# Kernel optimization log

Measured on AMD Instinct MI355X. Metric: run time of the kernel, lower is better.

The kernel has to match this reference:

```python
import jax, jax.numpy as jnp
import numpy as np

IN_FEATURES = 2048
OUT_FEATURES = 8192


def setup_inputs() -> dict:
    key = jax.random.key(0)
    k_x, k_w, k_s, k_b = jax.random.split(key, 4)
    x = jax.random.normal(k_x, (4, 2048, IN_FEATURES), dtype=jnp.float32)
    # int8 weights as produced by quantize(): values in [-128, 127]
    weight_int8 = jax.random.randint(k_w, (OUT_FEATURES, IN_FEATURES), -128, 128, dtype=jnp.int8)
    # per-output-row scale, shape [out_features, 1]
    scale = jax.random.uniform(k_s, (OUT_FEATURES, 1), dtype=jnp.float32, minval=1e-4, maxval=0.02)
    bias = jax.random.normal(k_b, (OUT_FEATURES,), dtype=jnp.float32) * 0.01
    return {"x": x, "weight_int8": weight_int8, "scale": scale, "bias": bias}


def reference(x, weight_int8, scale, bias):
    # dequantize: [out, in] int8 -> x.dtype, scaled per output row
    weight = weight_int8.astype(x.dtype) * scale.astype(x.dtype)
    # F.linear: x @ weight.T + bias
    return jnp.einsum('bsi,oi->bso', x, weight) + bias.astype(x.dtype)
```

## Files before the change

kernel.cpp:

```cpp
#include <hip/hip_runtime.h>
#include <hip/hip_bf16.h>

#define M_DIM 8192
#define N_DIM 8192
#define K_DIM 2048

#define BK 64
#define NT (K_DIM / BK)
#define SLOT_BYTES 32768

typedef float f32x4 __attribute__((ext_vector_type(4)));
typedef int   i32x4 __attribute__((ext_vector_type(4)));
typedef unsigned int u32;
typedef u32 u32x2 __attribute__((ext_vector_type(2)));
typedef u32 u32x4 __attribute__((ext_vector_type(4)));


__device__ __forceinline__ void gload16(const unsigned char* g, char* l) {
    __builtin_amdgcn_global_load_lds(
        (const __attribute__((address_space(1))) u32*)g,
        (__attribute__((address_space(3))) u32*)l, 16, 0, 0);
}

__device__ __forceinline__ u32 pack4(int a, int b, int c, int d) {
    return (u32)(a & 255) | ((u32)(b & 255) << 8) |
           ((u32)(c & 255) << 16) | ((u32)(d & 255) << 24);
}


__global__ void __launch_bounds__(256) quant_x_k(const float* __restrict__ x,
                                                 unsigned char* __restrict__ xq,
                                                 float* __restrict__ sx) {
    const int row = blockIdx.x;
    const int t = threadIdx.x;
    const float* xr = x + (size_t)row * K_DIM;
    f32x4 v0 = *((const f32x4*)xr + t * 2);
    f32x4 v1 = *((const f32x4*)xr + t * 2 + 1);
    float m = fabsf(v0[0]);
    m = fmaxf(m, fabsf(v0[1])); m = fmaxf(m, fabsf(v0[2])); m = fmaxf(m, fabsf(v0[3]));
    m = fmaxf(m, fabsf(v1[0])); m = fmaxf(m, fabsf(v1[1]));
    m = fmaxf(m, fabsf(v1[2])); m = fmaxf(m, fabsf(v1[3]));
#pragma unroll
    for (int off = 32; off >= 1; off >>= 1)
        m = fmaxf(m, __shfl_xor(m, off, 64));
    __shared__ float wmax[4];
    if ((t & 63) == 0) wmax[t >> 6] = m;
    __syncthreads();
    m = fmaxf(fmaxf(wmax[0], wmax[1]), fmaxf(wmax[2], wmax[3]));
    m = fmaxf(m, 1e-20f);
    const float rs = 127.0f / m;
    const int q0 = (int)rintf(v0[0] * rs), q1 = (int)rintf(v0[1] * rs);
    const int q2 = (int)rintf(v0[2] * rs), q3 = (int)rintf(v0[3] * rs);
    const int q4 = (int)rintf(v1[0] * rs), q5 = (int)rintf(v1[1] * rs);
    const int q6 = (int)rintf(v1[2] * rs), q7 = (int)rintf(v1[3] * rs);
    u32x2 o;
    o[0] = pack4(q0, q1, q2, q3);
    o[1] = pack4(q4, q5, q6, q7);
    *((u32x2*)(xq + (size_t)row * K_DIM) + t) = o;
    if (t == 0) sx[row] = m / 127.0f;
}


__global__ void __launch_bounds__(256) cvt_w_k(const int* __restrict__ w,
                                               unsigned char* __restrict__ wq, int n16) {
    const int stride = gridDim.x * blockDim.x;
    for (int i = blockIdx.x * blockDim.x + threadIdx.x; i < n16; i += stride) {
        const i32x4* p = (const i32x4*)w + (size_t)i * 4;
        i32x4 a = p[0], b = p[1], c = p[2], d = p[3];
        u32x4 o;
        o[0] = pack4(a[0], a[1], a[2], a[3]);
        o[1] = pack4(b[0], b[1], b[2], b[3]);
        o[2] = pack4(c[0], c[1], c[2], c[3]);
        o[3] = pack4(d[0], d[1], d[2], d[3]);
        *((u32x4*)wq + i) = o;
    }
}


__global__ void __launch_bounds__(512, 2)
gemm_i8(const unsigned char* __restrict__ Aq, const unsigned char* __restrict__ Bq,
        const float* __restrict__ sx, const float* __restrict__ sw,
        const float* __restrict__ bias, float* __restrict__ C) {
    extern __shared__ __align__(16) char ldsb[];

    const int bid = blockIdx.x;
    const int swz = (bid & 7) * 128 + (bid >> 3);
    const int rowBase = (swz >> 5) * 256;
    const int colBase = (swz & 31) * 256;

    const int t = threadIdx.x;
    const int l = t & 63;
    const int w = t >> 6;
    const int wm = w >> 2;
    const int wn = w & 3;
    const int fr = l & 15;
    const int s4 = l >> 4;

    const int sr = t >> 2;
    const int sk = (((t & 3) ^ ((sr >> 1) & 3)) * 16);
    const unsigned char* gA0 = Aq + (size_t)(rowBase + sr) * K_DIM + sk;
    const unsigned char* gA1 = Aq + (size_t)(rowBase + 128 + sr) * K_DIM + sk;
    const unsigned char* gB0 = Bq + (size_t)(colBase + sr) * K_DIM + sk;
    const unsigned char* gB1 = Bq + (size_t)(colBase + 128 + sr) * K_DIM + sk;

#define STAGE(tk) do { \
        char* _b = ldsb + ((tk) & 3) * SLOT_BYTES; \
        const int _k = (tk) * BK; \
        gload16(gA0 + _k, _b + t * 16); \
        gload16(gA1 + _k, _b + 8192 + t * 16); \
        gload16(gB0 + _k, _b + 16384 + t * 16); \
        gload16(gB1 + _k, _b + 24576 + t * 16); \
    } while (0)

    const int pc = ((s4 ^ ((fr >> 1) & 3)) * 16);
    int aoff[8], boff[4];
#pragma unroll
    for (int mi = 0; mi < 8; ++mi)
        aoff[mi] = (wm * 128 + mi * 16 + fr) * 64 + pc;
#pragma unroll
    for (int ni = 0; ni < 4; ++ni)
        boff[ni] = 16384 + (wn * 64 + ni * 16 + fr) * 64 + pc;

    i32x4 acc[8][4] = {};
    i32x4 af0[8], bf0[4], af1[8], bf1[4];

#define SB    __builtin_amdgcn_sched_barrier(0)
#define BAR   __builtin_amdgcn_s_barrier()
#define P1    __builtin_amdgcn_s_setprio(1)
#define P0    __builtin_amdgcn_s_setprio(0)
#define LGKM0 asm volatile("s_waitcnt lgkmcnt(0)" ::: "memory")
#define VM4   asm volatile("s_waitcnt vmcnt(4)" ::: "memory")
#define VM0   asm volatile("s_waitcnt vmcnt(0)" ::: "memory")

#define READS(T, AF, BF) do { \
        const char* _s = ldsb + ((T) & 3) * SLOT_BYTES; \
        _Pragma("unroll") \
        for (int mi = 0; mi < 8; ++mi) AF[mi] = *(const i32x4*)(_s + aoff[mi]); \
        _Pragma("unroll") \
        for (int ni = 0; ni < 4; ++ni) BF[ni] = *(const i32x4*)(_s + boff[ni]); \
    } while (0)

#define MFMA32(AF, BF) do { P1; \
        _Pragma("unroll") \
        for (int mi = 0; mi < 8; ++mi) \
            _Pragma("unroll") \
            for (int ni = 0; ni < 4; ++ni) \
                acc[mi][ni] = __builtin_amdgcn_mfma_i32_16x16x64_i8( \
                    AF[mi], BF[ni], acc[mi][ni], 0, 0, 0); \
        P0; } while (0)

#define BODY(T, AC, BC, AN, BN, DOSTAGE, VMW) do { \
        READS(T, AN, BN); \
        if (DOSTAGE) STAGE((T) + 2); \
        SB; \
        MFMA32(AC, BC); \
        VMW; LGKM0; SB; BAR; SB; \
    } while (0)

    STAGE(0); STAGE(1); STAGE(2);
    VM4; SB; BAR; SB;
    READS(0, af0, bf0);
    LGKM0; SB;

#pragma unroll
    for (int tt = 1; tt <= 27; tt += 2) {
        BODY(tt,     af0, bf0, af1, bf1, true, VM4);
        BODY(tt + 1, af1, bf1, af0, bf0, true, VM4);
    }
    BODY(29, af0, bf0, af1, bf1, true,  VM4);
    BODY(30, af1, bf1, af0, bf0, false, VM0);
    READS(31, af1, bf1);
    SB;
    MFMA32(af0, bf0);
    LGKM0; SB;
    MFMA32(af1, bf1);

#undef BODY
#undef MFMA32
#undef READS
#undef STAGE

#pragma unroll
    for (int ni = 0; ni < 4; ++ni) {
        const int col = colBase + wn * 64 + ni * 16 + fr;
        const float swc = sw[col];
        const float bz = bias[col];
#pragma unroll
        for (int mi = 0; mi < 8; ++mi) {
            const int rb = rowBase + wm * 128 + mi * 16 + s4 * 4;
            i32x4 a = acc[mi][ni];
#pragma unroll
            for (int r = 0; r < 4; ++r)
                C[(size_t)(rb + r) * N_DIM + col] =
                    (float)a[r] * (sx[rb + r] * swc) + bz;
        }
    }
}


typedef int i32x4_t __attribute__((ext_vector_type(4)));
__global__ void __launch_bounds__(256) naive_k(const float* __restrict__ x,
                                               const int* __restrict__ w,
                                               const float* __restrict__ scale,
                                               const float* __restrict__ bias,
                                               float* __restrict__ out) {
    __shared__ float xs[K_DIM];
    const int m = blockIdx.x >> 5;
    const int n = ((blockIdx.x & 31) << 8) + threadIdx.x;
    for (int i = threadIdx.x; i < K_DIM; i += 256) xs[i] = x[(size_t)m * K_DIM + i];
    __syncthreads();
    const int* wr = w + (size_t)n * K_DIM;
    float acc = 0.f;
    for (int k = 0; k < K_DIM; k += 4) {
        i32x4_t v = *(const i32x4_t*)(wr + k);
        acc += xs[k]     * (float)v[0];
        acc += xs[k + 1] * (float)v[1];
        acc += xs[k + 2] * (float)v[2];
        acc += xs[k + 3] * (float)v[3];
    }
    out[(size_t)m * N_DIM + n] = acc * scale[n] + bias[n];
}


extern "C" void kernel_launch(void* const* d_in, const int* in_sizes, int n_in,
                              void* d_out, int out_size, void* d_ws, size_t ws_size,
                              hipStream_t stream) {
    const float* x     = (const float*)d_in[0];
    const int*   w8    = (const int*)d_in[1];
    const float* sw    = (const float*)d_in[2];
    const float* bias  = (const float*)d_in[3];
    float*       out   = (float*)d_out;

    const size_t xq_bytes = (size_t)M_DIM * K_DIM;
    const size_t wq_bytes = (size_t)N_DIM * K_DIM;
    const size_t need = xq_bytes + wq_bytes + (size_t)M_DIM * sizeof(float);
    if (ws_size >= need) {
        unsigned char* xq = (unsigned char*)d_ws;
        unsigned char* wq = xq + xq_bytes;
        float* sx = (float*)(wq + wq_bytes);
        hipFuncSetAttribute((const void*)gemm_i8,
                            hipFuncAttributeMaxDynamicSharedMemorySize, 131072);
        quant_x_k<<<M_DIM, 256, 0, stream>>>(x, xq, sx);
        cvt_w_k<<<2048, 256, 0, stream>>>(w8, wq, N_DIM * K_DIM / 16);
        gemm_i8<<<dim3((M_DIM / 256) * (N_DIM / 256)), 512, 131072, stream>>>(
            xq, wq, sx, sw, bias, out);
    } else {
        naive_k<<<(M_DIM * (N_DIM / 256)), 256, 0, stream>>>(x, w8, sw, bias, out);
    }
}
```

Before: 235.9 us.

## Pre-swizzle operands into MFMA fragment layout and load directly to registers

The quantize and convert kernels now emit A and B in a per-16-row fragment-major layout, so each lane's MFMA operand is one contiguous 16-byte load. The GEMM drops the LDS staging, barriers and swizzled LDS reads, and instead double-buffers fragment loads from global memory straight into registers. This removes LDS traffic and synchronisation. The cost is that waves sharing rows or columns each re-fetch the same data, which raises L2/global traffic and exposes load latency.

```diff
diff --git a/kernel.cpp b/kernel.cpp
--- a/kernel.cpp
+++ b/kernel.cpp
@@ -7,20 +7,11 @@
 
 #define BK 64
 #define NT (K_DIM / BK)
-#define SLOT_BYTES 32768
 
 typedef float f32x4 __attribute__((ext_vector_type(4)));
 typedef int   i32x4 __attribute__((ext_vector_type(4)));
 typedef unsigned int u32;
-typedef u32 u32x2 __attribute__((ext_vector_type(2)));
 typedef u32 u32x4 __attribute__((ext_vector_type(4)));
-
-
-__device__ __forceinline__ void gload16(const unsigned char* g, char* l) {
-    __builtin_amdgcn_global_load_lds(
-        (const __attribute__((address_space(1))) u32*)g,
-        (__attribute__((address_space(3))) u32*)l, 16, 0, 0);
-}
 
 __device__ __forceinline__ u32 pack4(int a, int b, int c, int d) {
     return (u32)(a & 255) | ((u32)(b & 255) << 8) |
@@ -29,60 +20,76 @@
 
 
 __global__ void __launch_bounds__(256) quant_x_k(const float* __restrict__ x,
-                                                 unsigned char* __restrict__ xq,
+                                                 unsigned char* __restrict__ At,
                                                  float* __restrict__ sx) {
-    const int row = blockIdx.x;
+    const int g = blockIdx.x;
     const int t = threadIdx.x;
-    const float* xr = x + (size_t)row * K_DIM;
-    f32x4 v0 = *((const f32x4*)xr + t * 2);
-    f32x4 v1 = *((const f32x4*)xr + t * 2 + 1);
-    float m = fabsf(v0[0]);
-    m = fmaxf(m, fabsf(v0[1])); m = fmaxf(m, fabsf(v0[2])); m = fmaxf(m, fabsf(v0[3]));
-    m = fmaxf(m, fabsf(v1[0])); m = fmaxf(m, fabsf(v1[1]));
-    m = fmaxf(m, fabsf(v1[2])); m = fmaxf(m, fabsf(v1[3]));
-#pragma unroll
-    for (int off = 32; off >= 1; off >>= 1)
+    const int fr = t >> 4;
+    const int kc = t & 15;
+    const int row = g * 16 + fr;
+    const f32x4* xr = (const f32x4*)(x + (size_t)row * K_DIM + kc * 128);
+
+    f32x4 v[32];
+    float m = 0.f;
+#pragma unroll
+    for (int i = 0; i < 32; ++i) {
+        v[i] = xr[i];
+        m = fmaxf(m, fmaxf(fmaxf(fabsf(v[i][0]), fabsf(v[i][1])),
+                           fmaxf(fabsf(v[i][2]), fabsf(v[i][3]))));
+    }
+#pragma unroll
+    for (int off = 8; off >= 1; off >>= 1)
         m = fmaxf(m, __shfl_xor(m, off, 64));
-    __shared__ float wmax[4];
-    if ((t & 63) == 0) wmax[t >> 6] = m;
-    __syncthreads();
-    m = fmaxf(fmaxf(wmax[0], wmax[1]), fmaxf(wmax[2], wmax[3]));
     m = fmaxf(m, 1e-20f);
     const float rs = 127.0f / m;
-    const int q0 = (int)rintf(v0[0] * rs), q1 = (int)rintf(v0[1] * rs);
-    const int q2 = (int)rintf(v0[2] * rs), q3 = (int)rintf(v0[3] * rs);
-    const int q4 = (int)rintf(v1[0] * rs), q5 = (int)rintf(v1[1] * rs);
-    const int q6 = (int)rintf(v1[2] * rs), q7 = (int)rintf(v1[3] * rs);
-    u32x2 o;
-    o[0] = pack4(q0, q1, q2, q3);
-    o[1] = pack4(q4, q5, q6, q7);
-    *((u32x2*)(xq + (size_t)row * K_DIM) + t) = o;
-    if (t == 0) sx[row] = m / 127.0f;
+
+#pragma unroll
+    for (int kk = 0; kk < 8; ++kk) {
+        const int k = kc * 128 + kk * 16;
+        const int kt = k >> 6;
+        const int s4 = (k >> 4) & 3;
+        u32x4 o;
+#pragma unroll
+        for (int j = 0; j < 4; ++j) {
+            f32x4 f = v[kk * 4 + j];
+            o[j] = pack4((int)rintf(f[0] * rs), (int)rintf(f[1] * rs),
+                         (int)rintf(f[2] * rs), (int)rintf(f[3] * rs));
+        }
+        *(u32x4*)(At + (size_t)g * 32768 + kt * 1024 + (s4 * 16 + fr) * 16) = o;
+    }
+    if (kc == 0) sx[row] = m / 127.0f;
 }
 
 
 __global__ void __launch_bounds__(256) cvt_w_k(const int* __restrict__ w,
-                                               unsigned char* __restrict__ wq, int n16) {
-    const int stride = gridDim.x * blockDim.x;
-    for (int i = blockIdx.x * blockDim.x + threadIdx.x; i < n16; i += stride) {
-        const i32x4* p = (const i32x4*)w + (size_t)i * 4;
-        i32x4 a = p[0], b = p[1], c = p[2], d = p[3];
+                                               unsigned char* __restrict__ Bt) {
+    const int g = blockIdx.x;
+    const int t = threadIdx.x;
+    const int fr = t >> 4;
+    const int kc = t & 15;
+    const int col = g * 16 + fr;
+    const int* wr = w + (size_t)col * K_DIM + kc * 128;
+
+#pragma unroll
+    for (int kk = 0; kk < 8; ++kk) {
+        const int k = kc * 128 + kk * 16;
+        const int kt = k >> 6;
+        const int s4 = (k >> 4) & 3;
         u32x4 o;
-        o[0] = pack4(a[0], a[1], a[2], a[3]);
-        o[1] = pack4(b[0], b[1], b[2], b[3]);
-        o[2] = pack4(c[0], c[1], c[2], c[3]);
-        o[3] = pack4(d[0], d[1], d[2], d[3]);
-        *((u32x4*)wq + i) = o;
+#pragma unroll
+        for (int j = 0; j < 4; ++j) {
+            i32x4 a = *(const i32x4*)(wr + kk * 16 + j * 4);
+            o[j] = pack4(a[0], a[1], a[2], a[3]);
+        }
+        *(u32x4*)(Bt + (size_t)g * 32768 + kt * 1024 + (s4 * 16 + fr) * 16) = o;
     }
 }
 
 
 __global__ void __launch_bounds__(512, 2)
-gemm_i8(const unsigned char* __restrict__ Aq, const unsigned char* __restrict__ Bq,
+gemm_i8(const unsigned char* __restrict__ At, const unsigned char* __restrict__ Bt,
         const float* __restrict__ sx, const float* __restrict__ sw,
         const float* __restrict__ bias, float* __restrict__ C) {
-    extern __shared__ __align__(16) char ldsb[];
-
     const int bid = blockIdx.x;
     const int swz = (bid & 7) * 128 + (bid >> 3);
     const int rowBase = (swz >> 5) * 256;
@@ -96,48 +103,30 @@
     const int fr = l & 15;
     const int s4 = l >> 4;
 
-    const int sr = t >> 2;
-    const int sk = (((t & 3) ^ ((sr >> 1) & 3)) * 16);
-    const unsigned char* gA0 = Aq + (size_t)(rowBase + sr) * K_DIM + sk;
-    const unsigned char* gA1 = Aq + (size_t)(rowBase + 128 + sr) * K_DIM + sk;
-    const unsigned char* gB0 = Bq + (size_t)(colBase + sr) * K_DIM + sk;
-    const unsigned char* gB1 = Bq + (size_t)(colBase + 128 + sr) * K_DIM + sk;
-
-#define STAGE(tk) do { \
-        char* _b = ldsb + ((tk) & 3) * SLOT_BYTES; \
-        const int _k = (tk) * BK; \
-        gload16(gA0 + _k, _b + t * 16); \
-        gload16(gA1 + _k, _b + 8192 + t * 16); \
-        gload16(gB0 + _k, _b + 16384 + t * 16); \
-        gload16(gB1 + _k, _b + 24576 + t * 16); \
-    } while (0)
-
-    const int pc = ((s4 ^ ((fr >> 1) & 3)) * 16);
-    int aoff[8], boff[4];
+    const unsigned char* aB[8];
+    const unsigned char* bB[4];
 #pragma unroll
     for (int mi = 0; mi < 8; ++mi)
-        aoff[mi] = (wm * 128 + mi * 16 + fr) * 64 + pc;
+        aB[mi] = At + (size_t)(rowBase / 16 + wm * 8 + mi) * 32768 + l * 16;
 #pragma unroll
     for (int ni = 0; ni < 4; ++ni)
-        boff[ni] = 16384 + (wn * 64 + ni * 16 + fr) * 64 + pc;
+        bB[ni] = Bt + (size_t)(colBase / 16 + wn * 4 + ni) * 32768 + l * 16;
 
     i32x4 acc[8][4] = {};
-    i32x4 af0[8], bf0[4], af1[8], bf1[4];
-
-#define SB    __builtin_amdgcn_sched_barrier(0)
-#define BAR   __builtin_amdgcn_s_barrier()
+    i32x4 a0[8], b0[4], a1[8], b1[4];
+
 #define P1    __builtin_amdgcn_s_setprio(1)
 #define P0    __builtin_amdgcn_s_setprio(0)
-#define LGKM0 asm volatile("s_waitcnt lgkmcnt(0)" ::: "memory")
-#define VM4   asm volatile("s_waitcnt vmcnt(4)" ::: "memory")
+#define VM12  asm volatile("s_waitcnt vmcnt(12)" ::: "memory")
 #define VM0   asm volatile("s_waitcnt vmcnt(0)" ::: "memory")
 
-#define READS(T, AF, BF) do { \
-        const char* _s = ldsb + ((T) & 3) * SLOT_BYTES; \
+#define LOADT(T, AF, BF) do { \
         _Pragma("unroll") \
-        for (int mi = 0; mi < 8; ++mi) AF[mi] = *(const i32x4*)(_s + aoff[mi]); \
+        for (int mi = 0; mi < 8; ++mi) \
+            AF[mi] = *(const i32x4*)(aB[mi] + (T) * 1024); \
         _Pragma("unroll") \
-        for (int ni = 0; ni < 4; ++ni) BF[ni] = *(const i32x4*)(_s + boff[ni]); \
+        for (int ni = 0; ni < 4; ++ni) \
+            BF[ni] = *(const i32x4*)(bB[ni] + (T) * 1024); \
     } while (0)
 
 #define MFMA32(AF, BF) do { P1; \
@@ -149,36 +138,22 @@
                     AF[mi], BF[ni], acc[mi][ni], 0, 0, 0); \
         P0; } while (0)
 
-#define BODY(T, AC, BC, AN, BN, DOSTAGE, VMW) do { \
-        READS(T, AN, BN); \
-        if (DOSTAGE) STAGE((T) + 2); \
-        SB; \
-        MFMA32(AC, BC); \
-        VMW; LGKM0; SB; BAR; SB; \
-    } while (0)
-
-    STAGE(0); STAGE(1); STAGE(2);
-    VM4; SB; BAR; SB;
-    READS(0, af0, bf0);
-    LGKM0; SB;
-
-#pragma unroll
-    for (int tt = 1; tt <= 27; tt += 2) {
-        BODY(tt,     af0, bf0, af1, bf1, true, VM4);
-        BODY(tt + 1, af1, bf1, af0, bf0, true, VM4);
-    }
-    BODY(29, af0, bf0, af1, bf1, true,  VM4);
-    BODY(30, af1, bf1, af0, bf0, false, VM0);
-    READS(31, af1, bf1);
-    SB;
-    MFMA32(af0, bf0);
-    LGKM0; SB;
-    MFMA32(af1, bf1);
-
-#undef BODY
+    LOADT(0, a0, b0);
+#pragma unroll
+    for (int tt = 0; tt < NT; ++tt) {
+        if (tt + 1 < NT) {
+            if ((tt + 1) & 1) LOADT(tt + 1, a1, b1);
+            else              LOADT(tt + 1, a0, b0);
+            VM12;
+        } else {
+            VM0;
+        }
+        if (tt & 1) MFMA32(a1, b1);
+        else        MFMA32(a0, b0);
+    }
+
 #undef MFMA32
-#undef READS
-#undef STAGE
+#undef LOADT
 
 #pragma unroll
     for (int ni = 0; ni < 4; ++ni) {
@@ -235,15 +210,13 @@
     const size_t wq_bytes = (size_t)N_DIM * K_DIM;
     const size_t need = xq_bytes + wq_bytes + (size_t)M_DIM * sizeof(float);
     if (ws_size >= need) {
-        unsigned char* xq = (unsigned char*)d_ws;
-        unsigned char* wq = xq + xq_bytes;
-        float* sx = (float*)(wq + wq_bytes);
-        hipFuncSetAttribute((const void*)gemm_i8,
-                            hipFuncAttributeMaxDynamicSharedMemorySize, 131072);
-        quant_x_k<<<M_DIM, 256, 0, stream>>>(x, xq, sx);
-        cvt_w_k<<<2048, 256, 0, stream>>>(w8, wq, N_DIM * K_DIM / 16);
-        gemm_i8<<<dim3((M_DIM / 256) * (N_DIM / 256)), 512, 131072, stream>>>(
-            xq, wq, sx, sw, bias, out);
+        unsigned char* At = (unsigned char*)d_ws;
+        unsigned char* Bt = At + xq_bytes;
+        float* sx = (float*)(Bt + wq_bytes);
+        quant_x_k<<<M_DIM / 16, 256, 0, stream>>>(x, At, sx);
+        cvt_w_k<<<N_DIM / 16, 256, 0, stream>>>(w8, Bt);
+        gemm_i8<<<dim3((M_DIM / 256) * (N_DIM / 256)), 512, 0, stream>>>(
+            At, Bt, sx, sw, bias, out);
     } else {
         naive_k<<<(M_DIM * (N_DIM / 256)), 256, 0, stream>>>(x, w8, sw, bias, out);
     }
```

Result: slower. 327.6 us (+38.9%).

## Split K-tile into four MFMA quadrants interleaved with LDS reads, prefetch depth three

Applied to the files above, without the earlier changes.

Restructures the main loop so each K-tile's 32 MFMAs run as four 8-MFMA quadrants, with LDS fragment reads for the next quadrant or tile issued between them. The prefetch distance becomes three tiles ahead in the 4-slot LDS ring instead of two, with vmcnt waits adjusted to match. Fragment registers drop from double-buffered full sets to half-size A/B pieces, which lowers register pressure. The cost is many more workgroup barriers per tile and a non-unrolled loop, which adds synchronisation and loop overhead.

```diff
diff --git a/kernel.cpp b/kernel.cpp
--- a/kernel.cpp
+++ b/kernel.cpp
@@ -122,62 +122,68 @@
         boff[ni] = 16384 + (wn * 64 + ni * 16 + fr) * 64 + pc;
 
     i32x4 acc[8][4] = {};
-    i32x4 af0[8], bf0[4], af1[8], bf1[4];
+    i32x4 aLo[4], aHi[4], bLo[2], bHi[2];
 
 #define SB    __builtin_amdgcn_sched_barrier(0)
 #define BAR   __builtin_amdgcn_s_barrier()
 #define P1    __builtin_amdgcn_s_setprio(1)
-#define P0    __builtin_amdgcn_s_setprio(0)
+#define P0p   __builtin_amdgcn_s_setprio(0)
 #define LGKM0 asm volatile("s_waitcnt lgkmcnt(0)" ::: "memory")
+#define VM8   asm volatile("s_waitcnt vmcnt(8)" ::: "memory")
 #define VM4   asm volatile("s_waitcnt vmcnt(4)" ::: "memory")
 #define VM0   asm volatile("s_waitcnt vmcnt(0)" ::: "memory")
-
-#define READS(T, AF, BF) do { \
-        const char* _s = ldsb + ((T) & 3) * SLOT_BYTES; \
-        _Pragma("unroll") \
-        for (int mi = 0; mi < 8; ++mi) AF[mi] = *(const i32x4*)(_s + aoff[mi]); \
-        _Pragma("unroll") \
-        for (int ni = 0; ni < 4; ++ni) BF[ni] = *(const i32x4*)(_s + boff[ni]); \
+#define VMNOP do {} while (0)
+
+#define RD_ALO(T) do { const char* _s = ldsb + ((T) & 3) * SLOT_BYTES; \
+        _Pragma("unroll") \
+        for (int i = 0; i < 4; ++i) aLo[i] = *(const i32x4*)(_s + aoff[i]); } while (0)
+#define RD_AHI(T) do { const char* _s = ldsb + ((T) & 3) * SLOT_BYTES; \
+        _Pragma("unroll") \
+        for (int i = 0; i < 4; ++i) aHi[i] = *(const i32x4*)(_s + aoff[4 + i]); } while (0)
+#define RD_BLO(T) do { const char* _s = ldsb + ((T) & 3) * SLOT_BYTES; \
+        _Pragma("unroll") \
+        for (int i = 0; i < 2; ++i) bLo[i] = *(const i32x4*)(_s + boff[i]); } while (0)
+#define RD_BHI(T) do { const char* _s = ldsb + ((T) & 3) * SLOT_BYTES; \
+        _Pragma("unroll") \
+        for (int i = 0; i < 2; ++i) bHi[i] = *(const i32x4*)(_s + boff[2 + i]); } while (0)
+
+#define MM8(AF, BF, MO, NO) do { P1; \
+        _Pragma("unroll") \
+        for (int mi = 0; mi < 4; ++mi) \
+            _Pragma("unroll") \
+            for (int ni = 0; ni < 2; ++ni) \
+                acc[(MO) + mi][(NO) + ni] = __builtin_amdgcn_mfma_i32_16x16x64_i8( \
+                    AF[mi], BF[ni], acc[(MO) + mi][(NO) + ni], 0, 0, 0); \
+        P0p; } while (0)
+
+#define TILE8(T, DOSTG, VMW, RDNXT) do { \
+         RD_BHI(T); if (DOSTG) STAGE((T) + 3); \
+        SB; BAR; LGKM0; SB; MM8(aLo, bLo, 0, 0); SB; BAR; \
+         RD_AHI(T); VMW; \
+        SB; BAR; LGKM0; SB; MM8(aLo, bHi, 0, 2); SB; BAR; \
+         if (RDNXT) RD_ALO((T) + 1); \
+        SB; BAR; LGKM0; SB; MM8(aHi, bLo, 4, 0); SB; BAR; \
+         if (RDNXT) RD_BLO((T) + 1); \
+        SB; BAR; LGKM0; SB; MM8(aHi, bHi, 4, 2); SB; BAR; \
     } while (0)
 
-#define MFMA32(AF, BF) do { P1; \
-        _Pragma("unroll") \
-        for (int mi = 0; mi < 8; ++mi) \
-            _Pragma("unroll") \
-            for (int ni = 0; ni < 4; ++ni) \
-                acc[mi][ni] = __builtin_amdgcn_mfma_i32_16x16x64_i8( \
-                    AF[mi], BF[ni], acc[mi][ni], 0, 0, 0); \
-        P0; } while (0)
-
-#define BODY(T, AC, BC, AN, BN, DOSTAGE, VMW) do { \
-        READS(T, AN, BN); \
-        if (DOSTAGE) STAGE((T) + 2); \
-        SB; \
-        MFMA32(AC, BC); \
-        VMW; LGKM0; SB; BAR; SB; \
-    } while (0)
-
     STAGE(0); STAGE(1); STAGE(2);
-    VM4; SB; BAR; SB;
-    READS(0, af0, bf0);
-    LGKM0; SB;
-
-#pragma unroll
-    for (int tt = 1; tt <= 27; tt += 2) {
-        BODY(tt,     af0, bf0, af1, bf1, true, VM4);
-        BODY(tt + 1, af1, bf1, af0, bf0, true, VM4);
-    }
-    BODY(29, af0, bf0, af1, bf1, true,  VM4);
-    BODY(30, af1, bf1, af0, bf0, false, VM0);
-    READS(31, af1, bf1);
-    SB;
-    MFMA32(af0, bf0);
-    LGKM0; SB;
-    MFMA32(af1, bf1);
-
-#undef BODY
-#undef MFMA32
-#undef READS
+    VM8; SB; BAR; SB;
+    RD_ALO(0); RD_BLO(0);
+
+#pragma unroll 1
+    for (int T = 0; T < NT - 3; ++T)
+        TILE8(T, true, VM8, true);
+    TILE8(NT - 3, false, VM4, true);
+    TILE8(NT - 2, false, VM0, true);
+    TILE8(NT - 1, false, VMNOP, false);
+
+#undef TILE8
+#undef MM8
+#undef RD_ALO
+#undef RD_AHI
+#undef RD_BLO
+#undef RD_BHI
 #undef STAGE
 
 #pragma unroll
```

Result: no change. 232.4 us (-1.5%).

## Restructure int8 GEMM main loop to BK=128 double buffer with interleaved quarter-tile pipeline

Applied to the files above, without the earlier changes.

The int8 MFMA GEMM now uses a 128-wide K tile with two 64KB LDS buffers instead of four 32KB slots at BK=64. Each K tile is processed in four M-quarters, and A-fragment reads, B-fragment reads and global-to-LDS staging are interleaved with the MFMA groups, using finer lgkmcnt/vmcnt waits and an 8-way XOR swizzle. The aim is to halve the number of outer iterations and overlap LDS reads and global loads with matrix math more tightly. In exchange there are many more barriers per tile, and the larger LDS footprint may limit occupancy.

```diff
diff --git a/kernel.cpp b/kernel.cpp
--- a/kernel.cpp
+++ b/kernel.cpp
@@ -5,9 +5,9 @@
 #define N_DIM 8192
 #define K_DIM 2048
 
-#define BK 64
+#define BK 128
 #define NT (K_DIM / BK)
-#define SLOT_BYTES 32768
+#define BUF_BYTES 65536
 
 typedef float f32x4 __attribute__((ext_vector_type(4)));
 typedef int   i32x4 __attribute__((ext_vector_type(4)));
@@ -49,13 +49,11 @@
     m = fmaxf(fmaxf(wmax[0], wmax[1]), fmaxf(wmax[2], wmax[3]));
     m = fmaxf(m, 1e-20f);
     const float rs = 127.0f / m;
-    const int q0 = (int)rintf(v0[0] * rs), q1 = (int)rintf(v0[1] * rs);
-    const int q2 = (int)rintf(v0[2] * rs), q3 = (int)rintf(v0[3] * rs);
-    const int q4 = (int)rintf(v1[0] * rs), q5 = (int)rintf(v1[1] * rs);
-    const int q6 = (int)rintf(v1[2] * rs), q7 = (int)rintf(v1[3] * rs);
     u32x2 o;
-    o[0] = pack4(q0, q1, q2, q3);
-    o[1] = pack4(q4, q5, q6, q7);
+    o[0] = pack4((int)rintf(v0[0] * rs), (int)rintf(v0[1] * rs),
+                 (int)rintf(v0[2] * rs), (int)rintf(v0[3] * rs));
+    o[1] = pack4((int)rintf(v1[0] * rs), (int)rintf(v1[1] * rs),
+                 (int)rintf(v1[2] * rs), (int)rintf(v1[3] * rs));
     *((u32x2*)(xq + (size_t)row * K_DIM) + t) = o;
     if (t == 0) sx[row] = m / 127.0f;
 }
@@ -96,89 +94,112 @@
     const int fr = l & 15;
     const int s4 = l >> 4;
 
-    const int sr = t >> 2;
-    const int sk = (((t & 3) ^ ((sr >> 1) & 3)) * 16);
-    const unsigned char* gA0 = Aq + (size_t)(rowBase + sr) * K_DIM + sk;
-    const unsigned char* gA1 = Aq + (size_t)(rowBase + 128 + sr) * K_DIM + sk;
-    const unsigned char* gB0 = Bq + (size_t)(colBase + sr) * K_DIM + sk;
-    const unsigned char* gB1 = Bq + (size_t)(colBase + 128 + sr) * K_DIM + sk;
-
-#define STAGE(tk) do { \
-        char* _b = ldsb + ((tk) & 3) * SLOT_BYTES; \
-        const int _k = (tk) * BK; \
-        gload16(gA0 + _k, _b + t * 16); \
-        gload16(gA1 + _k, _b + 8192 + t * 16); \
-        gload16(gB0 + _k, _b + 16384 + t * 16); \
-        gload16(gB1 + _k, _b + 24576 + t * 16); \
+    const int sr = t >> 3;
+    const int sk = ((t & 7) ^ (sr & 7)) * 16;
+    const unsigned char* gA = Aq + (size_t)(rowBase + sr) * K_DIM + sk;
+    const unsigned char* gB = Bq + (size_t)(colBase + sr) * K_DIM + sk;
+
+#define STG_A(BUF, H, TK) do { \
+        const unsigned char* _s = gA + (size_t)((H) * 128) * K_DIM + (TK) * BK; \
+        gload16(_s, ldsb + (BUF) + (H) * 16384 + t * 16); \
+        gload16(_s + (size_t)64 * K_DIM, ldsb + (BUF) + (H) * 16384 + 8192 + t * 16); \
     } while (0)
-
-    const int pc = ((s4 ^ ((fr >> 1) & 3)) * 16);
-    int aoff[8], boff[4];
-#pragma unroll
-    for (int mi = 0; mi < 8; ++mi)
-        aoff[mi] = (wm * 128 + mi * 16 + fr) * 64 + pc;
-#pragma unroll
-    for (int ni = 0; ni < 4; ++ni)
-        boff[ni] = 16384 + (wn * 64 + ni * 16 + fr) * 64 + pc;
+#define STG_B(BUF, H, TK) do { \
+        const unsigned char* _s = gB + (size_t)((H) * 128) * K_DIM + (TK) * BK; \
+        gload16(_s, ldsb + (BUF) + 32768 + (H) * 16384 + t * 16); \
+        gload16(_s + (size_t)64 * K_DIM, ldsb + (BUF) + 32768 + (H) * 16384 + 8192 + t * 16); \
+    } while (0)
+
+    const int pc0 = ((0 + s4) ^ (fr & 7)) * 16;
+    const int pc1 = ((4 + s4) ^ (fr & 7)) * 16;
+    const int aBase = wm * 16384 + fr * 128;
+    const int bBase = 32768 + (wn * 64 + fr) * 128;
+
+#define RD_AQ(DST, BUF, MQ) do { \
+        const char* _p = ldsb + (BUF) + aBase + (MQ) * 4096; \
+        DST[0] = *(const i32x4*)(_p + pc0); \
+        DST[1] = *(const i32x4*)(_p + pc1); \
+        DST[2] = *(const i32x4*)(_p + 2048 + pc0); \
+        DST[3] = *(const i32x4*)(_p + 2048 + pc1); \
+    } while (0)
+#define RD_BALL(DST, BUF) do { \
+        const char* _p = ldsb + (BUF) + bBase; \
+        _Pragma("unroll") \
+        for (int ni = 0; ni < 4; ++ni) { \
+            DST[ni * 2 + 0] = *(const i32x4*)(_p + ni * 2048 + pc0); \
+            DST[ni * 2 + 1] = *(const i32x4*)(_p + ni * 2048 + pc1); \
+        } } while (0)
 
     i32x4 acc[8][4] = {};
-    i32x4 af0[8], bf0[4], af1[8], bf1[4];
+    i32x4 aQa[4], aQb[4], bC[8], bN[8];
 
 #define SB    __builtin_amdgcn_sched_barrier(0)
 #define BAR   __builtin_amdgcn_s_barrier()
 #define P1    __builtin_amdgcn_s_setprio(1)
-#define P0    __builtin_amdgcn_s_setprio(0)
-#define LGKM0 asm volatile("s_waitcnt lgkmcnt(0)" ::: "memory")
-#define VM4   asm volatile("s_waitcnt vmcnt(4)" ::: "memory")
+#define P0p   __builtin_amdgcn_s_setprio(0)
+#define LG4   asm volatile("s_waitcnt lgkmcnt(4)" ::: "memory")
+#define LG12  asm volatile("s_waitcnt lgkmcnt(12)" ::: "memory")
+#define LG0   asm volatile("s_waitcnt lgkmcnt(0)" ::: "memory")
+#define VM2   asm volatile("s_waitcnt vmcnt(2)" ::: "memory")
 #define VM0   asm volatile("s_waitcnt vmcnt(0)" ::: "memory")
 
-#define READS(T, AF, BF) do { \
-        const char* _s = ldsb + ((T) & 3) * SLOT_BYTES; \
+#define MM16(MQ, AQ, B) do { P1; \
         _Pragma("unroll") \
-        for (int mi = 0; mi < 8; ++mi) AF[mi] = *(const i32x4*)(_s + aoff[mi]); \
-        _Pragma("unroll") \
-        for (int ni = 0; ni < 4; ++ni) BF[ni] = *(const i32x4*)(_s + boff[ni]); \
-    } while (0)
-
-#define MFMA32(AF, BF) do { P1; \
-        _Pragma("unroll") \
-        for (int mi = 0; mi < 8; ++mi) \
+        for (int mi2 = 0; mi2 < 2; ++mi2) \
             _Pragma("unroll") \
             for (int ni = 0; ni < 4; ++ni) \
-                acc[mi][ni] = __builtin_amdgcn_mfma_i32_16x16x64_i8( \
-                    AF[mi], BF[ni], acc[mi][ni], 0, 0, 0); \
-        P0; } while (0)
-
-#define BODY(T, AC, BC, AN, BN, DOSTAGE, VMW) do { \
-        READS(T, AN, BN); \
-        if (DOSTAGE) STAGE((T) + 2); \
-        SB; \
-        MFMA32(AC, BC); \
-        VMW; LGKM0; SB; BAR; SB; \
-    } while (0)
-
-    STAGE(0); STAGE(1); STAGE(2);
-    VM4; SB; BAR; SB;
-    READS(0, af0, bf0);
-    LGKM0; SB;
-
-#pragma unroll
-    for (int tt = 1; tt <= 27; tt += 2) {
-        BODY(tt,     af0, bf0, af1, bf1, true, VM4);
-        BODY(tt + 1, af1, bf1, af0, bf0, true, VM4);
-    }
-    BODY(29, af0, bf0, af1, bf1, true,  VM4);
-    BODY(30, af1, bf1, af0, bf0, false, VM0);
-    READS(31, af1, bf1);
-    SB;
-    MFMA32(af0, bf0);
-    LGKM0; SB;
-    MFMA32(af1, bf1);
-
-#undef BODY
-#undef MFMA32
-#undef READS
-#undef STAGE
+                _Pragma("unroll") \
+                for (int kk = 0; kk < 2; ++kk) \
+                    acc[(MQ) * 2 + mi2][ni] = __builtin_amdgcn_mfma_i32_16x16x64_i8( \
+                        AQ[mi2 * 2 + kk], B[ni * 2 + kk], acc[(MQ) * 2 + mi2][ni], 0, 0, 0); \
+        P0p; } while (0)
+
+    STG_A(0, 0, 0); STG_A(0, 1, 0); STG_B(0, 0, 0); STG_B(0, 1, 0);
+    STG_A(BUF_BYTES, 0, 1);
+    VM2; SB; BAR; SB;
+    RD_AQ(aQa, 0, 0); RD_BALL(bC, 0);
+
+#pragma unroll 1
+    for (int T = 0; T < NT - 2; T += 2) {
+         RD_AQ(aQb, 0, 1); STG_A(BUF_BYTES, 1, T + 1);
+               SB; BAR; LG4; SB; MM16(0, aQa, bC); SB; BAR;
+         RD_AQ(aQa, 0, 2); STG_B(BUF_BYTES, 0, T + 1);
+               SB; BAR; LG4; SB; MM16(1, aQb, bC); SB; VM2; BAR;
+         RD_AQ(aQb, 0, 3); STG_B(BUF_BYTES, 1, T + 1);
+               SB; BAR; LG4; SB; MM16(2, aQa, bC); SB; VM0; BAR;
+         RD_BALL(bN, BUF_BYTES); RD_AQ(aQa, BUF_BYTES, 0); STG_A(0, 0, T + 2);
+               SB; BAR; LG12; SB; MM16(3, aQb, bC); SB; BAR;
+         RD_AQ(aQb, BUF_BYTES, 1); STG_A(0, 1, T + 2);
+               SB; BAR; LG4; SB; MM16(0, aQa, bN); SB; BAR;
+         RD_AQ(aQa, BUF_BYTES, 2); STG_B(0, 0, T + 2);
+               SB; BAR; LG4; SB; MM16(1, aQb, bN); SB; VM2; BAR;
+         RD_AQ(aQb, BUF_BYTES, 3); STG_B(0, 1, T + 2);
+               SB; BAR; LG4; SB; MM16(2, aQa, bN); SB; VM0; BAR;
+         RD_BALL(bC, 0); RD_AQ(aQa, 0, 0); STG_A(BUF_BYTES, 0, T + 3);
+               SB; BAR; LG12; SB; MM16(3, aQb, bN); SB; BAR;
+    }
+
+     RD_AQ(aQb, 0, 1); STG_A(BUF_BYTES, 1, NT - 1);
+           SB; BAR; LG4; SB; MM16(0, aQa, bC); SB; BAR;
+     RD_AQ(aQa, 0, 2); STG_B(BUF_BYTES, 0, NT - 1);
+           SB; BAR; LG4; SB; MM16(1, aQb, bC); SB; VM2; BAR;
+     RD_AQ(aQb, 0, 3); STG_B(BUF_BYTES, 1, NT - 1);
+           SB; BAR; LG4; SB; MM16(2, aQa, bC); SB; VM0; BAR;
+     RD_BALL(bN, BUF_BYTES); RD_AQ(aQa, BUF_BYTES, 0);
+           SB; BAR; LG12; SB; MM16(3, aQb, bC); SB; BAR;
+     RD_AQ(aQb, BUF_BYTES, 1);
+           SB; BAR; LG4; SB; MM16(0, aQa, bN); SB; BAR;
+     RD_AQ(aQa, BUF_BYTES, 2);
+           SB; BAR; LG4; SB; MM16(1, aQb, bN); SB; BAR;
+     RD_AQ(aQb, BUF_BYTES, 3);
+           SB; BAR; LG4; SB; MM16(2, aQa, bN); SB; BAR;
+     LG0; SB; MM16(3, aQb, bN);
+
+#undef MM16
+#undef RD_AQ
+#undef RD_BALL
+#undef STG_A
+#undef STG_B
 
 #pragma unroll
     for (int ni = 0; ni < 4; ++ni) {
```

New measurement: 287.4 us. 1.22x slower.
